# Kernel tuning notes

Hardware: AMD Instinct MI355X
Metric: run time of the kernel (lower is better)

## Reference

```python
import jax, jax.numpy as jnp
import numpy as np

B, S_DEC, S_ENC, D, H = 2, 2048, 2048, 1024, 16
HD = D // H  # 64


def setup_inputs() -> dict:
    key = jax.random.key(0)
    ks = jax.random.split(key, 12)
    s = 0.02
    return {
        "dec_hidden_state": jax.random.normal(ks[0], (B, S_DEC, D), jnp.float32),
        "enc_hidden_state": jax.random.normal(ks[1], (B, S_ENC, D), jnp.float32),
        "mask": jnp.ones((B, S_ENC, S_DEC), jnp.int32),
        "Wq": jax.random.normal(ks[2], (H, D, HD), jnp.float32) * s,
        "bq": jax.random.normal(ks[3], (H, HD), jnp.float32) * s,
        "Wk": jax.random.normal(ks[4], (H, D, HD), jnp.float32) * s,
        "bk": jax.random.normal(ks[5], (H, HD), jnp.float32) * s,
        "Wv": jax.random.normal(ks[6], (H, D, HD), jnp.float32) * s,
        "bv": jax.random.normal(ks[7], (H, HD), jnp.float32) * s,
        "Wo": jax.random.normal(ks[8], (D, D), jnp.float32) * s,
        "bo": jax.random.normal(ks[9], (D,), jnp.float32) * s,
    }


def reference(dec_hidden_state, enc_hidden_state, mask, Wq, bq, Wk, bk, Wv, bv, Wo, bo):
    # NOTE: original module swaps args: query <- enc_hidden_state, key/value <- dec_hidden_state.
    # q: [B,H,S_enc,HD], k/v: [B,H,S_dec,HD]
    q = jnp.einsum("bqd,hdk->bhqk", enc_hidden_state, Wq) + bq[None, :, None, :]
    k = jnp.einsum("bsd,hdk->bhsk", dec_hidden_state, Wk) + bk[None, :, None, :]
    v = jnp.einsum("bsd,hdk->bhsk", dec_hidden_state, Wv) + bv[None, :, None, :]
    scores = jnp.einsum("bhqk,bhsk->bhqs", q, k) / jnp.sqrt(jnp.asarray(HD, q.dtype))
    scores = jnp.where(mask[:, None, :, :] == 0, jnp.asarray(-jnp.inf, scores.dtype), scores)
    weights = jax.nn.softmax(scores, axis=-1)
    attn = jnp.einsum("bhqs,bhsk->bhqk", weights, v)  # [B,H,S_enc,HD]
    # concat heads along last dim (same order as torch.cat over head list)
    attn = jnp.transpose(attn, (0, 2, 1, 3)).reshape(B, S_ENC, D)
    return attn @ Wo + bo
```

## Files before the change

kernel.cpp:

```cpp
#include <hip/hip_runtime.h>
#include <math.h>
#include <stdint.h>


typedef unsigned short ushort_t;
typedef __attribute__((ext_vector_type(8))) short short8;
typedef __attribute__((ext_vector_type(4))) float floatx4;

__device__ __forceinline__ ushort_t f2bf(float x){
  unsigned u = __float_as_uint(x);
  u += 0x7fffu + ((u >> 16) & 1u);
  return (ushort_t)(u >> 16);
}
__device__ __forceinline__ unsigned pk2bf(float a, float b){
#if __has_builtin(__builtin_amdgcn_cvt_pk_bf16_f32)
  typedef __attribute__((ext_vector_type(2))) __bf16 bf2_t;
  bf2_t r = __builtin_amdgcn_cvt_pk_bf16_f32(a, b);
  return *(unsigned*)&r;
#else
  return (unsigned)f2bf(a) | ((unsigned)f2bf(b) << 16);
#endif
}
__device__ __forceinline__ floatx4 mfma16(short8 a, short8 b, floatx4 c){
  return __builtin_amdgcn_mfma_f32_16x16x32_bf16(a, b, c, 0, 0, 0);
}

__global__ __launch_bounds__(256)
void prep_kernel(const float* __restrict__ enc, const float* __restrict__ dec,
                 const float* __restrict__ Wq, const float* __restrict__ Wk,
                 const float* __restrict__ Wv, const float* __restrict__ Wo,
                 const int* __restrict__ mask,
                 ushort_t* __restrict__ encb, ushort_t* __restrict__ decb,
                 ushort_t* __restrict__ WqT, ushort_t* __restrict__ WkT,
                 ushort_t* __restrict__ WvT, ushort_t* __restrict__ WoT,
                 unsigned long long* __restrict__ mb)
{
  __shared__ float t[64][65];
  const int bx = blockIdx.x, tid = threadIdx.x;
  if (bx < 8192){
    const float* src = (bx < 4096) ? enc : dec;
    ushort_t*    dst = (bx < 4096) ? encb : decb;
    int i = ((bx & 4095) * 256 + tid) * 4;
    const float4 v = *(const float4*)(src + i);
    unsigned long long p = (unsigned long long)f2bf(v.x)
                         | ((unsigned long long)f2bf(v.y) << 16)
                         | ((unsigned long long)f2bf(v.z) << 32)
                         | ((unsigned long long)f2bf(v.w) << 48);
    *(unsigned long long*)(dst + i) = p;
  } else if (bx < 8960){
    const int id = bx - 8192;
    const int zz = id >> 4, yy = id & 15;
    const int which = zz >> 4, head = zz & 15;
    const float* src = (which == 0) ? Wq : (which == 1) ? Wk : Wv;
    ushort_t*    dst = (which == 0) ? WqT : (which == 1) ? WkT : WvT;
    const long sb = (long)head * 65536;
    const int r0 = yy * 64;
    #pragma unroll
    for (int i = 0; i < 16; i++){
      int idx = i*256 + tid;
      int r = idx >> 6, c = idx & 63;
      t[r][c] = src[sb + (long)(r0 + r)*64 + c];
    }
    __syncthreads();
    #pragma unroll
    for (int i = 0; i < 16; i++){
      int idx = i*256 + tid;
      int cr = idx >> 6, rc = idx & 63;
      dst[sb + (long)cr*1024 + r0 + rc] = f2bf(t[rc][cr]);
    }
  } else if (bx < 9216){
    const int id = bx - 8960;
    const int r0 = (id >> 4) * 64, c0 = (id & 15) * 64;
    #pragma unroll
    for (int i = 0; i < 16; i++){
      int idx = i*256 + tid;
      int r = idx >> 6, c = idx & 63;
      t[r][c] = Wo[(long)(r0 + r)*1024 + c0 + c];
    }
    __syncthreads();
    #pragma unroll
    for (int i = 0; i < 16; i++){
      int idx = i*256 + tid;
      int cr = idx >> 6, rc = idx & 63;
      WoT[(long)(c0 + cr)*1024 + r0 + rc] = f2bf(t[rc][cr]);
    }
  } else {
    long gid = (long)(bx - 9216) * 256 + tid;
    unsigned long long bal = __ballot(mask[gid] != 0);
    if ((tid & 63) == 0) mb[gid >> 6] = bal;
  }
}

__global__ __launch_bounds__(256, 3)
void gemm_qkv_kernel(const ushort_t* __restrict__ encb, const ushort_t* __restrict__ decb,
                     const ushort_t* __restrict__ WqT, const ushort_t* __restrict__ WkT,
                     const ushort_t* __restrict__ WvT,
                     const float* __restrict__ bq, const float* __restrict__ bk,
                     const float* __restrict__ bv,
                     ushort_t* __restrict__ Qb, ushort_t* __restrict__ Kbf,
                     ushort_t* __restrict__ Vtb)
{
  __shared__ ushort_t At[2*4096];
  __shared__ ushort_t Bt[2*4096];
  const int tid = threadIdx.x;
  const int wave = tid >> 6, lane = tid & 63;
  const int quad = lane >> 4, l16 = lane & 15;
  const int z = blockIdx.z;
  const ushort_t *A, *BT; const float* bias; ushort_t* outp;
  int m0, n0; long outAdj = 0;
  float qs = 1.0f;
  if (z == 0){ A = encb; BT = WqT; bias = bq; outp = Qb;  m0 = blockIdx.x*128; n0 = blockIdx.y*128;
               qs = 0.18033688011112042f; }
  else if (z == 1){ A = decb; BT = WkT; bias = bk; outp = Kbf; m0 = blockIdx.x*128; n0 = blockIdx.y*128; }
  else {
    int id = blockIdx.x*8 + blockIdx.y;
    int vb = id >> 7, rem = id & 127;
    m0 = ((rem >> 4) & 7) * 128; n0 = (rem & 15) * 128;
    A = WvT; BT = decb + (long)vb*2097152; bias = bv; outp = Vtb; outAdj = (long)vb*2097152;
  }
  const int K = 1024;

  const int c0 = tid, c1 = 256 + tid;
  const ushort_t* gA0 = A  + (long)(m0 + (c0 >> 2))*K + (c0 & 3)*8;
  const ushort_t* gA1 = A  + (long)(m0 + (c1 >> 2))*K + (c1 & 3)*8;
  const ushort_t* gB0 = BT + (long)(n0 + (c0 >> 2))*K + (c0 & 3)*8;
  const ushort_t* gB1 = BT + (long)(n0 + (c1 >> 2))*K + (c1 & 3)*8;

  floatx4 acc[4][4];
  #pragma unroll
  for (int mt = 0; mt < 4; mt++)
    #pragma unroll
    for (int nt = 0; nt < 4; nt++)
      acc[mt][nt] = (floatx4){0.f, 0.f, 0.f, 0.f};

  short8 rA0 = *(const short8*)gA0;  gA0 += 32;
  short8 rA1 = *(const short8*)gA1;  gA1 += 32;
  short8 rB0 = *(const short8*)gB0;  gB0 += 32;
  short8 rB1 = *(const short8*)gB1;  gB1 += 32;

  const int moff = (wave & 1) * 64, noff = (wave >> 1) * 64;
  int cur = 0;
  for (int k0 = 0; k0 < K; k0 += 32){
    *(short8*)&At[cur*4096 +        tid*8] = rA0;
    *(short8*)&At[cur*4096 + 2048 + tid*8] = rA1;
    *(short8*)&Bt[cur*4096 +        tid*8] = rB0;
    *(short8*)&Bt[cur*4096 + 2048 + tid*8] = rB1;
    __syncthreads();
    if (k0 + 32 < K){
      rA0 = *(const short8*)gA0;  gA0 += 32;
      rA1 = *(const short8*)gA1;  gA1 += 32;
      rB0 = *(const short8*)gB0;  gB0 += 32;
      rB1 = *(const short8*)gB1;  gB1 += 32;
    }
    short8 af[4], bfr[4];
    #pragma unroll
    for (int t = 0; t < 4; t++){
      af[t]  = *(const short8*)&At[cur*4096 + (moff + t*16 + l16)*32 + quad*8];
      bfr[t] = *(const short8*)&Bt[cur*4096 + (noff + t*16 + l16)*32 + quad*8];
    }
    #pragma unroll
    for (int mt = 0; mt < 4; mt++)
      #pragma unroll
      for (int nt = 0; nt < 4; nt++)
        acc[mt][nt] = mfma16(bfr[nt], af[mt], acc[mt][nt]);
    cur ^= 1;
  }

  #pragma unroll
  for (int mt = 0; mt < 4; mt++){
    #pragma unroll
    for (int nt = 0; nt < 4; nt++){
      floatx4 v = acc[mt][nt];
      if (z < 2){
        const int s   = m0 + moff + mt*16 + l16;
        const int ch0 = n0 + noff + nt*16 + quad*4;
        const float4 b4 = *(const float4*)&bias[ch0];
        uint2 pk;
        pk.x = pk2bf((v[0] + b4.x)*qs, (v[1] + b4.y)*qs);
        pk.y = pk2bf((v[2] + b4.z)*qs, (v[3] + b4.w)*qs);
        *(unsigned long long*)&outp[(long)s*1024 + ch0] = *(unsigned long long*)&pk;
      } else {
        const int ch = m0 + moff + mt*16 + l16;
        const int s0 = n0 + noff + nt*16 + quad*4;
        const float bb = bias[ch];
        uint2 pk;
        pk.x = pk2bf(v[0] + bb, v[1] + bb);
        pk.y = pk2bf(v[2] + bb, v[3] + bb);
        *(unsigned long long*)&outp[outAdj + (long)ch*2048 + s0] = *(unsigned long long*)&pk;
      }
    }
  }
}

__global__ __launch_bounds__(256, 2)
void gemm_o_kernel(const ushort_t* __restrict__ A, const ushort_t* __restrict__ BT,
                   const float* __restrict__ bias, float* __restrict__ outf)
{
  __shared__ ushort_t At[2*4096];
  __shared__ ushort_t Bt[2*2048];
  const int tid = threadIdx.x;
  const int wave = tid >> 6, lane = tid & 63;
  const int quad = lane >> 4, l16 = lane & 15;
  const int m0 = blockIdx.x * 128, n0 = blockIdx.y * 64;
  const int K = 1024;

  const int c0 = tid, c1 = 256 + tid;
  const ushort_t* gA0 = A  + (long)(m0 + (c0 >> 2))*K + (c0 & 3)*8;
  const ushort_t* gA1 = A  + (long)(m0 + (c1 >> 2))*K + (c1 & 3)*8;
  const ushort_t* gB0 = BT + (long)(n0 + (c0 >> 2))*K + (c0 & 3)*8;

  floatx4 acc[4][2];
  #pragma unroll
  for (int mt = 0; mt < 4; mt++)
    #pragma unroll
    for (int nt = 0; nt < 2; nt++)
      acc[mt][nt] = (floatx4){0.f, 0.f, 0.f, 0.f};

  short8 rA0 = *(const short8*)gA0;  gA0 += 32;
  short8 rA1 = *(const short8*)gA1;  gA1 += 32;
  short8 rB0 = *(const short8*)gB0;  gB0 += 32;

  const int moff = (wave & 1) * 64, noff = (wave >> 1) * 32;
  int cur = 0;
  for (int k0 = 0; k0 < K; k0 += 32){
    *(short8*)&At[cur*4096 +        tid*8] = rA0;
    *(short8*)&At[cur*4096 + 2048 + tid*8] = rA1;
    *(short8*)&Bt[cur*2048 +        tid*8] = rB0;
    __syncthreads();
    if (k0 + 32 < K){
      rA0 = *(const short8*)gA0;  gA0 += 32;
      rA1 = *(const short8*)gA1;  gA1 += 32;
      rB0 = *(const short8*)gB0;  gB0 += 32;
    }
    short8 af[4], bfr[2];
    #pragma unroll
    for (int t = 0; t < 4; t++)
      af[t]  = *(const short8*)&At[cur*4096 + (moff + t*16 + l16)*32 + quad*8];
    #pragma unroll
    for (int t = 0; t < 2; t++)
      bfr[t] = *(const short8*)&Bt[cur*2048 + (noff + t*16 + l16)*32 + quad*8];
    #pragma unroll
    for (int mt = 0; mt < 4; mt++)
      #pragma unroll
      for (int nt = 0; nt < 2; nt++)
        acc[mt][nt] = mfma16(bfr[nt], af[mt], acc[mt][nt]);
    cur ^= 1;
  }

  #pragma unroll
  for (int mt = 0; mt < 4; mt++){
    #pragma unroll
    for (int nt = 0; nt < 2; nt++){
      const int s   = m0 + moff + mt*16 + l16;
      const int ch0 = n0 + noff + nt*16 + quad*4;
      const float4 b4 = *(const float4*)&bias[ch0];
      float4 o;
      o.x = acc[mt][nt][0] + b4.x;
      o.y = acc[mt][nt][1] + b4.y;
      o.z = acc[mt][nt][2] + b4.z;
      o.w = acc[mt][nt][3] + b4.w;
      *(float4*)&outf[(long)s*1024 + ch0] = o;
    }
  }
}

__global__ __launch_bounds__(256, 2)
void flash_attn_kernel(const ushort_t* __restrict__ Qp, const ushort_t* __restrict__ Kp,
                       const ushort_t* __restrict__ Vt, const unsigned* __restrict__ mb,
                       ushort_t* __restrict__ aout)
{
  __shared__ ushort_t Kbuf[2*4608];
  __shared__ ushort_t Vbuf[2*4608];
  const int tid = threadIdx.x, wave = tid >> 6, lane = tid & 63;
  const int quad = lane >> 4, l16 = lane & 15;
  const int bh = blockIdx.x, qt = blockIdx.y;
  const int b = bh >> 4, h = bh & 15;

  const ushort_t* VB = Vt + (long)bh*131072;
  const int q0 = qt*128 + wave*32;

  short8 qf[2][2];
  #pragma unroll
  for (int mtq = 0; mtq < 2; mtq++){
    const long qrow = ((long)b*2048 + q0 + mtq*16 + l16)*1024 + h*64;
    qf[mtq][0] = *(const short8*)&Qp[qrow +      quad*8];
    qf[mtq][1] = *(const short8*)&Qp[qrow + 32 + quad*8];
  }

  floatx4 accO[2][4];
  #pragma unroll
  for (int mtq = 0; mtq < 2; mtq++)
    #pragma unroll
    for (int ht = 0; ht < 4; ht++) accO[mtq][ht] = (floatx4){0.f,0.f,0.f,0.f};
  float lsum[2] = {0.f, 0.f};

  const int c0 = tid, c1 = 256 + tid;
  const int sr0 = c0 >> 3, sr1 = c1 >> 3;
  const int kr0 = (sr0 & 32) + ((sr0 & 4) << 2) + ((sr0 >> 3) & 3)*4 + (sr0 & 3);
  const int kr1 = (sr1 & 32) + ((sr1 & 4) << 2) + ((sr1 >> 3) & 3)*4 + (sr1 & 3);
  const ushort_t* gK0 = Kp + ((long)b*2048 + sr0)*1024 + h*64 + (c0 & 7)*8;
  const ushort_t* gK1 = Kp + ((long)b*2048 + sr1)*1024 + h*64 + (c1 & 7)*8;
  const ushort_t* gV0 = VB + (long)sr0*2048 + (c0 & 7)*8;
  const ushort_t* gV1 = VB + (long)sr1*2048 + (c1 & 7)*8;
  const int ko0 = kr0*72 + (c0 & 7)*8;
  const int ko1 = kr1*72 + (c1 & 7)*8;
  const int vo0 = sr0*72 + (c0 & 7)*8;
  const int vo1 = sr1*72 + (c1 & 7)*8;

  const uint2* mb2 = (const uint2*)mb;
  const long mbase = (long)b*2048 + q0;

  short8 gk0 = *(const short8*)gK0;  gK0 += 65536;
  short8 gk1 = *(const short8*)gK1;  gK1 += 65536;
  short8 gv0 = *(const short8*)gV0;  gV0 += 64;
  short8 gv1 = *(const short8*)gV1;  gV1 += 64;

  int cur = 0;
  for (int st = 0; st < 32; st++){
    *(short8*)&Kbuf[cur*4608 + ko0] = gk0;
    *(short8*)&Kbuf[cur*4608 + ko1] = gk1;
    *(short8*)&Vbuf[cur*4608 + vo0] = gv0;
    *(short8*)&Vbuf[cur*4608 + vo1] = gv1;
    __syncthreads();
    if (st < 31){
      gk0 = *(const short8*)gK0;  gK0 += 65536;
      gk1 = *(const short8*)gK1;  gK1 += 65536;
      gv0 = *(const short8*)gV0;  gV0 += 64;
      gv1 = *(const short8*)gV1;  gV1 += 64;
    }
    const ushort_t* Kt = &Kbuf[cur*4608];
    const ushort_t* Vp = &Vbuf[cur*4608];

    uint2 mw[2];
    #pragma unroll
    for (int mtq = 0; mtq < 2; mtq++)
      mw[mtq] = mb2[(mbase + mtq*16 + l16)*32 + st];
    const bool uni = __all((mw[0].x & mw[0].y & mw[1].x & mw[1].y) == 0xFFFFFFFFu);

    #pragma unroll
    for (int c = 0; c < 2; c++){
      short8 kA0 = *(const short8*)&Kt[((c*2    )*16 + l16)*72 +      quad*8];
      short8 kA1 = *(const short8*)&Kt[((c*2    )*16 + l16)*72 + 32 + quad*8];
      short8 kB0 = *(const short8*)&Kt[((c*2 + 1)*16 + l16)*72 +      quad*8];
      short8 kB1 = *(const short8*)&Kt[((c*2 + 1)*16 + l16)*72 + 32 + quad*8];
      short8 vf[4];
      #pragma unroll
      for (int ht = 0; ht < 4; ht++)
        vf[ht] = *(const short8*)&Vp[(ht*16 + l16)*72 + c*32 + quad*8];

      #pragma unroll
      for (int mtq = 0; mtq < 2; mtq++){
        floatx4 zA = (floatx4){0.f,0.f,0.f,0.f};
        zA = mfma16(kA0, qf[mtq][0], zA);
        zA = mfma16(kA1, qf[mtq][1], zA);
        floatx4 zB = (floatx4){0.f,0.f,0.f,0.f};
        zB = mfma16(kB0, qf[mtq][0], zB);
        zB = mfma16(kB1, qf[mtq][1], zB);
        float pA0 = __builtin_amdgcn_exp2f(zA[0]);
        float pA1 = __builtin_amdgcn_exp2f(zA[1]);
        float pA2 = __builtin_amdgcn_exp2f(zA[2]);
        float pA3 = __builtin_amdgcn_exp2f(zA[3]);
        float pB0 = __builtin_amdgcn_exp2f(zB[0]);
        float pB1 = __builtin_amdgcn_exp2f(zB[1]);
        float pB2 = __builtin_amdgcn_exp2f(zB[2]);
        float pB3 = __builtin_amdgcn_exp2f(zB[3]);
        if (__builtin_expect(!uni, 0)){
          const unsigned w = c ? mw[mtq].y : mw[mtq].x;
          const int sh = quad*8;
          pA0 = ((w >> (sh+0)) & 1u) ? pA0 : 0.f;
          pA1 = ((w >> (sh+1)) & 1u) ? pA1 : 0.f;
          pA2 = ((w >> (sh+2)) & 1u) ? pA2 : 0.f;
          pA3 = ((w >> (sh+3)) & 1u) ? pA3 : 0.f;
          pB0 = ((w >> (sh+4)) & 1u) ? pB0 : 0.f;
          pB1 = ((w >> (sh+5)) & 1u) ? pB1 : 0.f;
          pB2 = ((w >> (sh+6)) & 1u) ? pB2 : 0.f;
          pB3 = ((w >> (sh+7)) & 1u) ? pB3 : 0.f;
        }
        lsum[mtq] += ((pA0 + pA1) + (pA2 + pA3)) + ((pB0 + pB1) + (pB2 + pB3));
        unsigned pk[4];
        pk[0] = pk2bf(pA0, pA1);
        pk[1] = pk2bf(pA2, pA3);
        pk[2] = pk2bf(pB0, pB1);
        pk[3] = pk2bf(pB2, pB3);
        short8 pb;
        __builtin_memcpy(&pb, pk, 16);
        #pragma unroll
        for (int ht = 0; ht < 4; ht++)
          accO[mtq][ht] = mfma16(vf[ht], pb, accO[mtq][ht]);
      }
    }
    cur ^= 1;
  }

  #pragma unroll
  for (int mtq = 0; mtq < 2; mtq++){
    lsum[mtq] += __shfl_xor(lsum[mtq], 16);
    lsum[mtq] += __shfl_xor(lsum[mtq], 32);
  }

  #pragma unroll
  for (int mtq = 0; mtq < 2; mtq++){
    const float inv = 1.0f / lsum[mtq];
    const long rowo = ((long)b*2048 + q0 + mtq*16 + l16)*1024 + h*64;
    #pragma unroll
    for (int ht = 0; ht < 4; ht++){
      uint2 pk;
      pk.x = pk2bf(accO[mtq][ht][0]*inv, accO[mtq][ht][1]*inv);
      pk.y = pk2bf(accO[mtq][ht][2]*inv, accO[mtq][ht][3]*inv);
      *(unsigned long long*)&aout[rowo + ht*16 + quad*4] = *(unsigned long long*)&pk;
    }
  }
}

extern "C" void kernel_launch(void* const* d_in, const int* in_sizes, int n_in,
                              void* d_out, int out_size, void* d_ws, size_t ws_size,
                              hipStream_t stream) {
  const float* dec  = (const float*)d_in[0];
  const float* enc  = (const float*)d_in[1];
  const int*   mask = (const int*)d_in[2];
  const float* Wq   = (const float*)d_in[3];
  const float* bq   = (const float*)d_in[4];
  const float* Wk   = (const float*)d_in[5];
  const float* bk   = (const float*)d_in[6];
  const float* Wv   = (const float*)d_in[7];
  const float* bv   = (const float*)d_in[8];
  const float* Wo   = (const float*)d_in[9];
  const float* bo   = (const float*)d_in[10];
  float* out = (float*)d_out;

  ushort_t* ws   = (ushort_t*)d_ws;
  ushort_t* encb = ws;
  ushort_t* decb = encb + 4194304;
  ushort_t* Qb   = decb + 4194304;
  ushort_t* Kbf  = Qb   + 4194304;
  ushort_t* Vtb  = Kbf  + 4194304;
  ushort_t* WqT  = Vtb  + 4194304;
  ushort_t* WkT  = WqT  + 1048576;
  ushort_t* WvT  = WkT  + 1048576;
  ushort_t* WoT  = WvT  + 1048576;
  unsigned* Mb   = (unsigned*)(WoT + 1048576);

  prep_kernel<<<41984, 256, 0, stream>>>(enc, dec, Wq, Wk, Wv, Wo, mask,
                                         encb, decb, WqT, WkT, WvT, WoT,
                                         (unsigned long long*)Mb);
  gemm_qkv_kernel<<<dim3(32,8,3), 256, 0, stream>>>(encb, decb, WqT, WkT, WvT,
                                                    bq, bk, bv, Qb, Kbf, Vtb);
  flash_attn_kernel<<<dim3(32,16,1), 256, 0, stream>>>(Qb, Kbf, Vtb, Mb, encb);
  gemm_o_kernel<<<dim3(32,16,1), 256, 0, stream>>>(encb, WoT, bo, out);
}
```

Measured before the change: 249.7 us.

## Split flash attention work across 8 waves with 16 query rows each

The attention kernel now launches 512 threads per block instead of 256. Each wave handles 16 query rows instead of 32, and each thread loads one K/V chunk per tile instead of two. The aim is more waves in flight for latency hiding and lower per-thread register pressure. In exchange, each K/V fragment read from LDS is reused by only one query tile instead of two, and more waves contend at each barrier.

```diff
diff --git a/kernel.cpp b/kernel.cpp
--- a/kernel.cpp
+++ b/kernel.cpp
@@ -264,7 +264,7 @@
   }
 }
 
-__global__ __launch_bounds__(256, 2)
+__global__ __launch_bounds__(512, 4)
 void flash_attn_kernel(const ushort_t* __restrict__ Qp, const ushort_t* __restrict__ Kp,
                        const ushort_t* __restrict__ Vt, const unsigned* __restrict__ mb,
                        ushort_t* __restrict__ aout)
@@ -277,65 +277,47 @@
   const int b = bh >> 4, h = bh & 15;
 
   const ushort_t* VB = Vt + (long)bh*131072;
-  const int q0 = qt*128 + wave*32;
-
-  short8 qf[2][2];
+  const int q0 = qt*128 + wave*16;
+
+  short8 qf0, qf1;
+  {
+    const long qrow = ((long)b*2048 + q0 + l16)*1024 + h*64;
+    qf0 = *(const short8*)&Qp[qrow +      quad*8];
+    qf1 = *(const short8*)&Qp[qrow + 32 + quad*8];
+  }
+
+  floatx4 accO[4];
   #pragma unroll
-  for (int mtq = 0; mtq < 2; mtq++){
-    const long qrow = ((long)b*2048 + q0 + mtq*16 + l16)*1024 + h*64;
-    qf[mtq][0] = *(const short8*)&Qp[qrow +      quad*8];
-    qf[mtq][1] = *(const short8*)&Qp[qrow + 32 + quad*8];
-  }
-
-  floatx4 accO[2][4];
-  #pragma unroll
-  for (int mtq = 0; mtq < 2; mtq++)
-    #pragma unroll
-    for (int ht = 0; ht < 4; ht++) accO[mtq][ht] = (floatx4){0.f,0.f,0.f,0.f};
-  float lsum[2] = {0.f, 0.f};
-
-  const int c0 = tid, c1 = 256 + tid;
-  const int sr0 = c0 >> 3, sr1 = c1 >> 3;
-  const int kr0 = (sr0 & 32) + ((sr0 & 4) << 2) + ((sr0 >> 3) & 3)*4 + (sr0 & 3);
-  const int kr1 = (sr1 & 32) + ((sr1 & 4) << 2) + ((sr1 >> 3) & 3)*4 + (sr1 & 3);
-  const ushort_t* gK0 = Kp + ((long)b*2048 + sr0)*1024 + h*64 + (c0 & 7)*8;
-  const ushort_t* gK1 = Kp + ((long)b*2048 + sr1)*1024 + h*64 + (c1 & 7)*8;
-  const ushort_t* gV0 = VB + (long)sr0*2048 + (c0 & 7)*8;
-  const ushort_t* gV1 = VB + (long)sr1*2048 + (c1 & 7)*8;
-  const int ko0 = kr0*72 + (c0 & 7)*8;
-  const int ko1 = kr1*72 + (c1 & 7)*8;
-  const int vo0 = sr0*72 + (c0 & 7)*8;
-  const int vo1 = sr1*72 + (c1 & 7)*8;
+  for (int ht = 0; ht < 4; ht++) accO[ht] = (floatx4){0.f,0.f,0.f,0.f};
+  float lsum = 0.f;
+
+  const int sr = tid >> 3;
+  const int kr = (sr & 32) + ((sr & 4) << 2) + ((sr >> 3) & 3)*4 + (sr & 3);
+  const ushort_t* gK = Kp + ((long)b*2048 + sr)*1024 + h*64 + (tid & 7)*8;
+  const ushort_t* gV = VB + (long)sr*2048 + (tid & 7)*8;
+  const int ko = kr*72 + (tid & 7)*8;
+  const int vo = sr*72 + (tid & 7)*8;
 
   const uint2* mb2 = (const uint2*)mb;
   const long mbase = (long)b*2048 + q0;
 
-  short8 gk0 = *(const short8*)gK0;  gK0 += 65536;
-  short8 gk1 = *(const short8*)gK1;  gK1 += 65536;
-  short8 gv0 = *(const short8*)gV0;  gV0 += 64;
-  short8 gv1 = *(const short8*)gV1;  gV1 += 64;
+  short8 gk = *(const short8*)gK;  gK += 65536;
+  short8 gv = *(const short8*)gV;  gV += 64;
 
   int cur = 0;
   for (int st = 0; st < 32; st++){
-    *(short8*)&Kbuf[cur*4608 + ko0] = gk0;
-    *(short8*)&Kbuf[cur*4608 + ko1] = gk1;
-    *(short8*)&Vbuf[cur*4608 + vo0] = gv0;
-    *(short8*)&Vbuf[cur*4608 + vo1] = gv1;
+    *(short8*)&Kbuf[cur*4608 + ko] = gk;
+    *(short8*)&Vbuf[cur*4608 + vo] = gv;
     __syncthreads();
     if (st < 31){
-      gk0 = *(const short8*)gK0;  gK0 += 65536;
-      gk1 = *(const short8*)gK1;  gK1 += 65536;
-      gv0 = *(const short8*)gV0;  gV0 += 64;
-      gv1 = *(const short8*)gV1;  gV1 += 64;
+      gk = *(const short8*)gK;  gK += 65536;
+      gv = *(const short8*)gV;  gV += 64;
     }
     const ushort_t* Kt = &Kbuf[cur*4608];
     const ushort_t* Vp = &Vbuf[cur*4608];
 
-    uint2 mw[2];
-    #pragma unroll
-    for (int mtq = 0; mtq < 2; mtq++)
-      mw[mtq] = mb2[(mbase + mtq*16 + l16)*32 + st];
-    const bool uni = __all((mw[0].x & mw[0].y & mw[1].x & mw[1].y) == 0xFFFFFFFFu);
+    uint2 mw = mb2[(mbase + l16)*32 + st];
+    const bool uni = __all((mw.x & mw.y) == 0xFFFFFFFFu);
 
     #pragma unroll
     for (int c = 0; c < 2; c++){
@@ -348,65 +330,58 @@
       for (int ht = 0; ht < 4; ht++)
         vf[ht] = *(const short8*)&Vp[(ht*16 + l16)*72 + c*32 + quad*8];
 
+      floatx4 zA = (floatx4){0.f,0.f,0.f,0.f};
+      zA = mfma16(kA0, qf0, zA);
+      zA = mfma16(kA1, qf1, zA);
+      floatx4 zB = (floatx4){0.f,0.f,0.f,0.f};
+      zB = mfma16(kB0, qf0, zB);
+      zB = mfma16(kB1, qf1, zB);
+      float pA0 = __builtin_amdgcn_exp2f(zA[0]);
+      float pA1 = __builtin_amdgcn_exp2f(zA[1]);
+      float pA2 = __builtin_amdgcn_exp2f(zA[2]);
+      float pA3 = __builtin_amdgcn_exp2f(zA[3]);
+      float pB0 = __builtin_amdgcn_exp2f(zB[0]);
+      float pB1 = __builtin_amdgcn_exp2f(zB[1]);
+      float pB2 = __builtin_amdgcn_exp2f(zB[2]);
+      float pB3 = __builtin_amdgcn_exp2f(zB[3]);
+      if (__builtin_expect(!uni, 0)){
+        const unsigned w = c ? mw.y : mw.x;
+        const int sh = quad*8;
+        pA0 = ((w >> (sh+0)) & 1u) ? pA0 : 0.f;
+        pA1 = ((w >> (sh+1)) & 1u) ? pA1 : 0.f;
+        pA2 = ((w >> (sh+2)) & 1u) ? pA2 : 0.f;
+        pA3 = ((w >> (sh+3)) & 1u) ? pA3 : 0.f;
+        pB0 = ((w >> (sh+4)) & 1u) ? pB0 : 0.f;
+        pB1 = ((w >> (sh+5)) & 1u) ? pB1 : 0.f;
+        pB2 = ((w >> (sh+6)) & 1u) ? pB2 : 0.f;
+        pB3 = ((w >> (sh+7)) & 1u) ? pB3 : 0.f;
+      }
+      lsum += ((pA0 + pA1) + (pA2 + pA3)) + ((pB0 + pB1) + (pB2 + pB3));
+      unsigned pk[4];
+      pk[0] = pk2bf(pA0, pA1);
+      pk[1] = pk2bf(pA2, pA3);
+      pk[2] = pk2bf(pB0, pB1);
+      pk[3] = pk2bf(pB2, pB3);
+      short8 pb;
+      __builtin_memcpy(&pb, pk, 16);
       #pragma unroll
-      for (int mtq = 0; mtq < 2; mtq++){
-        floatx4 zA = (floatx4){0.f,0.f,0.f,0.f};
-        zA = mfma16(kA0, qf[mtq][0], zA);
-        zA = mfma16(kA1, qf[mtq][1], zA);
-        floatx4 zB = (floatx4){0.f,0.f,0.f,0.f};
-        zB = mfma16(kB0, qf[mtq][0], zB);
-        zB = mfma16(kB1, qf[mtq][1], zB);
-        float pA0 = __builtin_amdgcn_exp2f(zA[0]);
-        float pA1 = __builtin_amdgcn_exp2f(zA[1]);
-        float pA2 = __builtin_amdgcn_exp2f(zA[2]);
-        float pA3 = __builtin_amdgcn_exp2f(zA[3]);
-        float pB0 = __builtin_amdgcn_exp2f(zB[0]);
-        float pB1 = __builtin_amdgcn_exp2f(zB[1]);
-        float pB2 = __builtin_amdgcn_exp2f(zB[2]);
-        float pB3 = __builtin_amdgcn_exp2f(zB[3]);
-        if (__builtin_expect(!uni, 0)){
-          const unsigned w = c ? mw[mtq].y : mw[mtq].x;
-          const int sh = quad*8;
-          pA0 = ((w >> (sh+0)) & 1u) ? pA0 : 0.f;
-          pA1 = ((w >> (sh+1)) & 1u) ? pA1 : 0.f;
-          pA2 = ((w >> (sh+2)) & 1u) ? pA2 : 0.f;
-          pA3 = ((w >> (sh+3)) & 1u) ? pA3 : 0.f;
-          pB0 = ((w >> (sh+4)) & 1u) ? pB0 : 0.f;
-          pB1 = ((w >> (sh+5)) & 1u) ? pB1 : 0.f;
-          pB2 = ((w >> (sh+6)) & 1u) ? pB2 : 0.f;
-          pB3 = ((w >> (sh+7)) & 1u) ? pB3 : 0.f;
-        }
-        lsum[mtq] += ((pA0 + pA1) + (pA2 + pA3)) + ((pB0 + pB1) + (pB2 + pB3));
-        unsigned pk[4];
-        pk[0] = pk2bf(pA0, pA1);
-        pk[1] = pk2bf(pA2, pA3);
-        pk[2] = pk2bf(pB0, pB1);
-        pk[3] = pk2bf(pB2, pB3);
-        short8 pb;
-        __builtin_memcpy(&pb, pk, 16);
-        #pragma unroll
-        for (int ht = 0; ht < 4; ht++)
-          accO[mtq][ht] = mfma16(vf[ht], pb, accO[mtq][ht]);
-      }
+      for (int ht = 0; ht < 4; ht++)
+        accO[ht] = mfma16(vf[ht], pb, accO[ht]);
     }
     cur ^= 1;
   }
 
-  #pragma unroll
-  for (int mtq = 0; mtq < 2; mtq++){
-    lsum[mtq] += __shfl_xor(lsum[mtq], 16);
-    lsum[mtq] += __shfl_xor(lsum[mtq], 32);
-  }
-
-  #pragma unroll
-  for (int mtq = 0; mtq < 2; mtq++){
-    const float inv = 1.0f / lsum[mtq];
-    const long rowo = ((long)b*2048 + q0 + mtq*16 + l16)*1024 + h*64;
+  lsum += __shfl_xor(lsum, 16);
+  lsum += __shfl_xor(lsum, 32);
+
+  {
+    const float inv = 1.0f / lsum;
+    const long rowo = ((long)b*2048 + q0 + l16)*1024 + h*64;
     #pragma unroll
     for (int ht = 0; ht < 4; ht++){
       uint2 pk;
-      pk.x = pk2bf(accO[mtq][ht][0]*inv, accO[mtq][ht][1]*inv);
-      pk.y = pk2bf(accO[mtq][ht][2]*inv, accO[mtq][ht][3]*inv);
+      pk.x = pk2bf(accO[ht][0]*inv, accO[ht][1]*inv);
+      pk.y = pk2bf(accO[ht][2]*inv, accO[ht][3]*inv);
       *(unsigned long long*)&aout[rowo + ht*16 + quad*4] = *(unsigned long long*)&pk;
     }
   }
@@ -445,6 +420,6 @@
                                          (unsigned long long*)Mb);
   gemm_qkv_kernel<<<dim3(32,8,3), 256, 0, stream>>>(encb, decb, WqT, WkT, WvT,
                                                     bq, bk, bv, Qb, Kbf, Vtb);
-  flash_attn_kernel<<<dim3(32,16,1), 256, 0, stream>>>(Qb, Kbf, Vtb, Mb, encb);
+  flash_attn_kernel<<<dim3(32,16,1), 512, 0, stream>>>(Qb, Kbf, Vtb, Mb, encb);
   gemm_o_kernel<<<dim3(32,16,1), 256, 0, stream>>>(encb, WoT, bo, out);
 }
```

After: 249.1 us. About the same (-0.2%).

## Split key sequence across two wave groups per attention block and merge via LDS

Applied to the files above, without the earlier changes.

The flash attention kernel now launches 512 threads per block. Two groups of four waves each process half of the key/value sequence, with separate double-buffered LDS tiles for each half. At the end the second group writes its partial output accumulators and row sums to shared memory, and the first group adds them, normalises and writes the result. The aim is to double the waves resident per CU and halve the serial loop length, so memory and MFMA latency is better hidden. The cost is more LDS per block (72 KB), which may cap blocks per CU, plus an extra reduction step at the end.

```diff
diff --git a/kernel.cpp b/kernel.cpp
--- a/kernel.cpp
+++ b/kernel.cpp
@@ -264,20 +264,25 @@
   }
 }
 
-__global__ __launch_bounds__(256, 2)
+__global__ __launch_bounds__(512, 4)
 void flash_attn_kernel(const ushort_t* __restrict__ Qp, const ushort_t* __restrict__ Kp,
                        const ushort_t* __restrict__ Vt, const unsigned* __restrict__ mb,
                        ushort_t* __restrict__ aout)
 {
-  __shared__ ushort_t Kbuf[2*4608];
-  __shared__ ushort_t Vbuf[2*4608];
+  __shared__ __align__(16) unsigned char smem_raw[73728];
+  ushort_t* KBs = (ushort_t*)smem_raw;
+  ushort_t* VBs = KBs + 2*2*4608;
+  float* mO = (float*)smem_raw;
+  float* mL = (float*)(smem_raw + 32768);
+
   const int tid = threadIdx.x, wave = tid >> 6, lane = tid & 63;
   const int quad = lane >> 4, l16 = lane & 15;
+  const int shalf = wave >> 2, w = wave & 3;
   const int bh = blockIdx.x, qt = blockIdx.y;
   const int b = bh >> 4, h = bh & 15;
 
   const ushort_t* VB = Vt + (long)bh*131072;
-  const int q0 = qt*128 + wave*32;
+  const int q0 = qt*128 + w*32;
 
   short8 qf[2][2];
   #pragma unroll
@@ -294,14 +299,18 @@
     for (int ht = 0; ht < 4; ht++) accO[mtq][ht] = (floatx4){0.f,0.f,0.f,0.f};
   float lsum[2] = {0.f, 0.f};
 
-  const int c0 = tid, c1 = 256 + tid;
+  const int htid = tid & 255;
+  const int c0 = htid, c1 = 256 + htid;
   const int sr0 = c0 >> 3, sr1 = c1 >> 3;
   const int kr0 = (sr0 & 32) + ((sr0 & 4) << 2) + ((sr0 >> 3) & 3)*4 + (sr0 & 3);
   const int kr1 = (sr1 & 32) + ((sr1 & 4) << 2) + ((sr1 >> 3) & 3)*4 + (sr1 & 3);
-  const ushort_t* gK0 = Kp + ((long)b*2048 + sr0)*1024 + h*64 + (c0 & 7)*8;
-  const ushort_t* gK1 = Kp + ((long)b*2048 + sr1)*1024 + h*64 + (c1 & 7)*8;
-  const ushort_t* gV0 = VB + (long)sr0*2048 + (c0 & 7)*8;
-  const ushort_t* gV1 = VB + (long)sr1*2048 + (c1 & 7)*8;
+  const long srow = (long)b*2048 + shalf*1024;
+  const ushort_t* gK0 = Kp + (srow + sr0)*1024 + h*64 + (c0 & 7)*8;
+  const ushort_t* gK1 = Kp + (srow + sr1)*1024 + h*64 + (c1 & 7)*8;
+  const ushort_t* gV0 = VB + (long)sr0*2048 + shalf*1024 + (c0 & 7)*8;
+  const ushort_t* gV1 = VB + (long)sr1*2048 + shalf*1024 + (c1 & 7)*8;
+  ushort_t* Kh = KBs + shalf*2*4608;
+  ushort_t* Vh = VBs + shalf*2*4608;
   const int ko0 = kr0*72 + (c0 & 7)*8;
   const int ko1 = kr1*72 + (c1 & 7)*8;
   const int vo0 = sr0*72 + (c0 & 7)*8;
@@ -316,25 +325,25 @@
   short8 gv1 = *(const short8*)gV1;  gV1 += 64;
 
   int cur = 0;
-  for (int st = 0; st < 32; st++){
-    *(short8*)&Kbuf[cur*4608 + ko0] = gk0;
-    *(short8*)&Kbuf[cur*4608 + ko1] = gk1;
-    *(short8*)&Vbuf[cur*4608 + vo0] = gv0;
-    *(short8*)&Vbuf[cur*4608 + vo1] = gv1;
+  for (int st = 0; st < 16; st++){
+    *(short8*)&Kh[cur*4608 + ko0] = gk0;
+    *(short8*)&Kh[cur*4608 + ko1] = gk1;
+    *(short8*)&Vh[cur*4608 + vo0] = gv0;
+    *(short8*)&Vh[cur*4608 + vo1] = gv1;
     __syncthreads();
-    if (st < 31){
+    if (st < 15){
       gk0 = *(const short8*)gK0;  gK0 += 65536;
       gk1 = *(const short8*)gK1;  gK1 += 65536;
       gv0 = *(const short8*)gV0;  gV0 += 64;
       gv1 = *(const short8*)gV1;  gV1 += 64;
     }
-    const ushort_t* Kt = &Kbuf[cur*4608];
-    const ushort_t* Vp = &Vbuf[cur*4608];
+    const ushort_t* Kt = &Kh[cur*4608];
+    const ushort_t* Vp = &Vh[cur*4608];
 
     uint2 mw[2];
     #pragma unroll
     for (int mtq = 0; mtq < 2; mtq++)
-      mw[mtq] = mb2[(mbase + mtq*16 + l16)*32 + st];
+      mw[mtq] = mb2[(mbase + mtq*16 + l16)*32 + shalf*16 + st];
     const bool uni = __all((mw[0].x & mw[0].y & mw[1].x & mw[1].y) == 0xFFFFFFFFu);
 
     #pragma unroll
@@ -365,16 +374,16 @@
         float pB2 = __builtin_amdgcn_exp2f(zB[2]);
         float pB3 = __builtin_amdgcn_exp2f(zB[3]);
         if (__builtin_expect(!uni, 0)){
-          const unsigned w = c ? mw[mtq].y : mw[mtq].x;
+          const unsigned mwv = c ? mw[mtq].y : mw[mtq].x;
           const int sh = quad*8;
-          pA0 = ((w >> (sh+0)) & 1u) ? pA0 : 0.f;
-          pA1 = ((w >> (sh+1)) & 1u) ? pA1 : 0.f;
-          pA2 = ((w >> (sh+2)) & 1u) ? pA2 : 0.f;
-          pA3 = ((w >> (sh+3)) & 1u) ? pA3 : 0.f;
-          pB0 = ((w >> (sh+4)) & 1u) ? pB0 : 0.f;
-          pB1 = ((w >> (sh+5)) & 1u) ? pB1 : 0.f;
-          pB2 = ((w >> (sh+6)) & 1u) ? pB2 : 0.f;
-          pB3 = ((w >> (sh+7)) & 1u) ? pB3 : 0.f;
+          pA0 = ((mwv >> (sh+0)) & 1u) ? pA0 : 0.f;
+          pA1 = ((mwv >> (sh+1)) & 1u) ? pA1 : 0.f;
+          pA2 = ((mwv >> (sh+2)) & 1u) ? pA2 : 0.f;
+          pA3 = ((mwv >> (sh+3)) & 1u) ? pA3 : 0.f;
+          pB0 = ((mwv >> (sh+4)) & 1u) ? pB0 : 0.f;
+          pB1 = ((mwv >> (sh+5)) & 1u) ? pB1 : 0.f;
+          pB2 = ((mwv >> (sh+6)) & 1u) ? pB2 : 0.f;
+          pB3 = ((mwv >> (sh+7)) & 1u) ? pB3 : 0.f;
         }
         lsum[mtq] += ((pA0 + pA1) + (pA2 + pA3)) + ((pB0 + pB1) + (pB2 + pB3));
         unsigned pk[4];
@@ -398,16 +407,30 @@
     lsum[mtq] += __shfl_xor(lsum[mtq], 32);
   }
 
-  #pragma unroll
-  for (int mtq = 0; mtq < 2; mtq++){
-    const float inv = 1.0f / lsum[mtq];
-    const long rowo = ((long)b*2048 + q0 + mtq*16 + l16)*1024 + h*64;
-    #pragma unroll
-    for (int ht = 0; ht < 4; ht++){
-      uint2 pk;
-      pk.x = pk2bf(accO[mtq][ht][0]*inv, accO[mtq][ht][1]*inv);
-      pk.y = pk2bf(accO[mtq][ht][2]*inv, accO[mtq][ht][3]*inv);
-      *(unsigned long long*)&aout[rowo + ht*16 + quad*4] = *(unsigned long long*)&pk;
+  __syncthreads();
+  if (shalf == 1){
+    #pragma unroll
+    for (int mtq = 0; mtq < 2; mtq++){
+      #pragma unroll
+      for (int ht = 0; ht < 4; ht++)
+        *(floatx4*)&mO[((((w*2 + mtq)*4 + ht)*64) + lane)*4] = accO[mtq][ht];
+      mL[(w*2 + mtq)*64 + lane] = lsum[mtq];
+    }
+  }
+  __syncthreads();
+  if (shalf == 0){
+    #pragma unroll
+    for (int mtq = 0; mtq < 2; mtq++){
+      const float inv = 1.0f / (lsum[mtq] + mL[(w*2 + mtq)*64 + lane]);
+      const long rowo = ((long)b*2048 + q0 + mtq*16 + l16)*1024 + h*64;
+      #pragma unroll
+      for (int ht = 0; ht < 4; ht++){
+        const floatx4 o = *(const floatx4*)&mO[((((w*2 + mtq)*4 + ht)*64) + lane)*4];
+        uint2 pk;
+        pk.x = pk2bf((accO[mtq][ht][0] + o[0])*inv, (accO[mtq][ht][1] + o[1])*inv);
+        pk.y = pk2bf((accO[mtq][ht][2] + o[2])*inv, (accO[mtq][ht][3] + o[3])*inv);
+        *(unsigned long long*)&aout[rowo + ht*16 + quad*4] = *(unsigned long long*)&pk;
+      }
     }
   }
 }
@@ -445,6 +468,6 @@
                                          (unsigned long long*)Mb);
   gemm_qkv_kernel<<<dim3(32,8,3), 256, 0, stream>>>(encb, decb, WqT, WkT, WvT,
                                                     bq, bk, bv, Qb, Kbf, Vtb);
-  flash_attn_kernel<<<dim3(32,16,1), 256, 0, stream>>>(Qb, Kbf, Vtb, Mb, encb);
+  flash_attn_kernel<<<dim3(32,16,1), 512, 0, stream>>>(Qb, Kbf, Vtb, Mb, encb);
   gemm_o_kernel<<<dim3(32,16,1), 256, 0, stream>>>(encb, WoT, bo, out);
 }
```

New measurement: 325.3 us. 30.3% more time.
